# Optimization experiments

Measured on AMD Instinct MI355X. Metric: run time of the kernel, lower is better.

The kernel has to match this reference:

```python
import jax, jax.numpy as jnp
import numpy as np

L = 10   # lattice side (hardcoded self.length)
K = 3    # kernel_size -> half_k = 1 wrap padding
FN = 4   # filter_num
B = 262144


def setup_inputs() -> dict:
    key = jax.random.key(0)
    k1, k2, k3, k4, k5 = jax.random.split(key, 5)
    v = jax.random.normal(k1, (B, L * L), dtype=jnp.float32)
    # torch default init scale ~ 1/sqrt(fan_in)
    conv_w = jax.random.normal(k2, (FN, 1, K, K), dtype=jnp.float32) / 3.0
    conv_b = jax.random.normal(k3, (FN,), dtype=jnp.float32) * 0.1
    deconv_w = jax.random.normal(k4, (FN, 1, 2, 2), dtype=jnp.float32) / 4.0
    deconv_b = jax.random.normal(k5, (1,), dtype=jnp.float32) * 0.1
    data = jnp.zeros((1,), dtype=jnp.int32)  # unused positional arg of log_psi
    return {"v": v, "conv_w": conv_w, "conv_b": conv_b,
            "deconv_w": deconv_w, "deconv_b": deconv_b, "data": data}


def _log_psi(v, conv_w, conv_b, deconv_w, deconv_b):
    b = v.shape[0]
    x = v.reshape(b, 1, L, L)
    # handmade_padding == periodic (wrap) pad of width half_k=1 on both spatial axes
    x = jnp.pad(x, ((0, 0), (0, 0), (1, 1), (1, 1)), mode="wrap")  # [B,1,12,12]
    # Conv2d(1, FN, 3), VALID -> [B,FN,10,10]
    y = jax.lax.conv_general_dilated(
        x, conv_w, window_strides=(1, 1), padding="VALID",
        dimension_numbers=("NCHW", "OIHW", "NCHW"))
    y = y + conv_b[None, :, None, None]
    # MaxPool2d(2,2): non-overlapping 2x2 -> [B,FN,5,5]
    y = y.reshape(b, FN, L // 2, 2, L // 2, 2).max(axis=(3, 5))
    # ConvTranspose2d(FN,1,kernel=2,stride=2): each input pixel -> disjoint 2x2 block
    # torch weight layout [in=FN, out=1, 2, 2]
    z = jnp.einsum("bcij,cokl->boikjl", y, deconv_w).reshape(b, 1, L, L)
    z = z + deconv_b[None, :, None, None]
    sign_z = jnp.sign(z)
    abs_z = z * sign_z
    sign_prod = sign_z.reshape(b, -1).prod(axis=1)        # scalar per sample
    log_sum = jnp.log(abs_z).reshape(b, -1).sum(axis=1)   # scalar per sample
    return sign_prod, log_sum


def reference(v, conv_w, conv_b, deconv_w, deconv_b, data):
    return _log_psi(v, conv_w, conv_b, deconv_w, deconv_b)
```

## Files before the change

kernel.cpp:

```cpp
#include <hip/hip_runtime.h>
#include <math.h>

__global__ __launch_bounds__(256) void CNN2D_37495064494620_kernel(
    const float* __restrict__ v,
    const float* __restrict__ cw,
    const float* __restrict__ cb,
    const float* __restrict__ dw,
    const float* __restrict__ db,
    float* __restrict__ out,
    int B)
{
    const int b = blockIdx.x * 256 + threadIdx.x;
    if (b >= B) return;

    float W[4][9];
    #pragma unroll
    for (int f = 0; f < 4; ++f)
        #pragma unroll
        for (int t = 0; t < 9; ++t)
            W[f][t] = cw[f * 9 + t];
    float Cb[4];
    #pragma unroll
    for (int f = 0; f < 4; ++f) Cb[f] = cb[f];
    float Dw[4][4];
    #pragma unroll
    for (int f = 0; f < 4; ++f)
        #pragma unroll
        for (int t = 0; t < 4; ++t)
            Dw[f][t] = dw[f * 4 + t];
    const float Db = db[0];

    float X[100];
    const float4* src = (const float4*)(v + (size_t)b * 100);
    #pragma unroll
    for (int t = 0; t < 25; ++t) {
        float4 q = src[t];
        X[4 * t + 0] = q.x;
        X[4 * t + 1] = q.y;
        X[4 * t + 2] = q.z;
        X[4 * t + 3] = q.w;
    }

    unsigned sbits = 0u;
    float l2 = 0.0f;

    #pragma unroll
    for (int i = 0; i < 5; ++i) {
        #pragma unroll
        for (int j = 0; j < 5; ++j) {
            float p0, p1, p2, p3;
            #pragma unroll
            for (int dr = 0; dr < 2; ++dr) {
                #pragma unroll
                for (int dc = 0; dc < 2; ++dc) {
                    const int r = 2 * i + dr, c = 2 * j + dc;
                    float a0 = Cb[0], a1 = Cb[1], a2 = Cb[2], a3 = Cb[3];
                    #pragma unroll
                    for (int kr = 0; kr < 3; ++kr) {
                        const int rr = (r + kr + 9) % 10;
                        #pragma unroll
                        for (int kc = 0; kc < 3; ++kc) {
                            const int cc = (c + kc + 9) % 10;
                            const float xv = X[rr * 10 + cc];
                            const int t = kr * 3 + kc;
                            a0 = fmaf(xv, W[0][t], a0);
                            a1 = fmaf(xv, W[1][t], a1);
                            a2 = fmaf(xv, W[2][t], a2);
                            a3 = fmaf(xv, W[3][t], a3);
                        }
                    }
                    if (dr == 0 && dc == 0) {
                        p0 = a0; p1 = a1; p2 = a2; p3 = a3;
                    } else {
                        p0 = fmaxf(p0, a0); p1 = fmaxf(p1, a1);
                        p2 = fmaxf(p2, a2); p3 = fmaxf(p3, a3);
                    }
                }
            }
            float z[4];
            #pragma unroll
            for (int kl = 0; kl < 4; ++kl) {
                float zz = Db;
                zz = fmaf(p0, Dw[0][kl], zz);
                zz = fmaf(p1, Dw[1][kl], zz);
                zz = fmaf(p2, Dw[2][kl], zz);
                zz = fmaf(p3, Dw[3][kl], zz);
                z[kl] = zz;
                sbits ^= __float_as_uint(zz);
            }
            l2 += __log2f(fabsf(z[0] * z[1])) + __log2f(fabsf(z[2] * z[3]));
        }
    }

    out[b]     = (sbits & 0x80000000u) ? -1.0f : 1.0f;
    out[B + b] = l2 * 0.69314718055994531f;
}

extern "C" void kernel_launch(void* const* d_in, const int* in_sizes, int n_in,
                              void* d_out, int out_size, void* d_ws, size_t ws_size,
                              hipStream_t stream) {
    const float* v  = (const float*)d_in[0];
    const float* cw = (const float*)d_in[1];
    const float* cb = (const float*)d_in[2];
    const float* dw = (const float*)d_in[3];
    const float* db = (const float*)d_in[4];
    float* out = (float*)d_out;

    const int B = in_sizes[0] / 100;
    const int grid = (B + 255) / 256;
    CNN2D_37495064494620_kernel<<<grid, 256, 0, stream>>>(v, cw, cb, dw, db, out, B);
}
```

Before: 171.3 us.

## Stream input rows in pairs and broadcast weights via readfirstlane

Instead of loading all 100 floats of a sample into registers up front, the kernel loads the lattice in 20-float row-pair chunks and processes one pooled row at a time. It reloads the second row-pair for the wrap-around so fewer values need to stay live at once. Weights and biases are passed through readfirstlane so they can sit in scalar registers instead of per-lane VGPRs. The aim is lower VGPR pressure and higher occupancy, at the cost of one redundant 80-byte global load per sample.

After: 174.1 us. No clear change (+1.6%).

```diff
diff --git a/kernel.cpp b/kernel.cpp
--- a/kernel.cpp
+++ b/kernel.cpp
@@ -1,5 +1,79 @@
 #include <hip/hip_runtime.h>
 #include <math.h>
+
+
+#define SREAD(x) __int_as_float(__builtin_amdgcn_readfirstlane(__float_as_int(x)))
+
+__device__ __forceinline__ void load_pair(float (&P)[20], const float* base) {
+    const float4* s = (const float4*)base;
+    #pragma unroll
+    for (int t = 0; t < 5; ++t) {
+        float4 q = s[t];
+        P[4 * t + 0] = q.x;
+        P[4 * t + 1] = q.y;
+        P[4 * t + 2] = q.z;
+        P[4 * t + 3] = q.w;
+    }
+}
+
+__device__ __forceinline__ void pool_row(
+    const float (&pa)[20], const float (&pb)[20], const float (&pc)[20],
+    const float (&W)[4][9], const float (&Cb)[4], const float (&Dw)[4][4],
+    const float Db, const int j2base ,
+    unsigned& sbits, float& l2)
+{
+    (void)j2base;
+    float Xw[4][10];
+    #pragma unroll
+    for (int c = 0; c < 10; ++c) {
+        Xw[0][c] = pa[10 + c];
+        Xw[1][c] = pb[c];
+        Xw[2][c] = pb[10 + c];
+        Xw[3][c] = pc[c];
+    }
+    #pragma unroll
+    for (int j = 0; j < 5; ++j) {
+        float p0, p1, p2, p3;
+        #pragma unroll
+        for (int dr = 0; dr < 2; ++dr) {
+            #pragma unroll
+            for (int dc = 0; dc < 2; ++dc) {
+                float a0 = Cb[0], a1 = Cb[1], a2 = Cb[2], a3 = Cb[3];
+                #pragma unroll
+                for (int kr = 0; kr < 3; ++kr) {
+                    #pragma unroll
+                    for (int kc = 0; kc < 3; ++kc) {
+                        const int cc = (2 * j + dc + kc + 9) % 10;
+                        const float xv = Xw[dr + kr][cc];
+                        const int t = kr * 3 + kc;
+                        a0 = fmaf(xv, W[0][t], a0);
+                        a1 = fmaf(xv, W[1][t], a1);
+                        a2 = fmaf(xv, W[2][t], a2);
+                        a3 = fmaf(xv, W[3][t], a3);
+                    }
+                }
+                if (dr == 0 && dc == 0) {
+                    p0 = a0; p1 = a1; p2 = a2; p3 = a3;
+                } else {
+                    p0 = fmaxf(p0, a0); p1 = fmaxf(p1, a1);
+                    p2 = fmaxf(p2, a2); p3 = fmaxf(p3, a3);
+                }
+            }
+        }
+        float z[4];
+        #pragma unroll
+        for (int kl = 0; kl < 4; ++kl) {
+            float zz = Db;
+            zz = fmaf(p0, Dw[0][kl], zz);
+            zz = fmaf(p1, Dw[1][kl], zz);
+            zz = fmaf(p2, Dw[2][kl], zz);
+            zz = fmaf(p3, Dw[3][kl], zz);
+            z[kl] = zz;
+            sbits ^= __float_as_uint(zz);
+        }
+        l2 += __log2f(fabsf(z[0] * z[1])) + __log2f(fabsf(z[2] * z[3]));
+    }
+}
 
 __global__ __launch_bounds__(256) void CNN2D_37495064494620_kernel(
     const float* __restrict__ v,
@@ -18,79 +92,43 @@
     for (int f = 0; f < 4; ++f)
         #pragma unroll
         for (int t = 0; t < 9; ++t)
-            W[f][t] = cw[f * 9 + t];
+            W[f][t] = SREAD(cw[f * 9 + t]);
     float Cb[4];
     #pragma unroll
-    for (int f = 0; f < 4; ++f) Cb[f] = cb[f];
+    for (int f = 0; f < 4; ++f) Cb[f] = SREAD(cb[f]);
     float Dw[4][4];
     #pragma unroll
     for (int f = 0; f < 4; ++f)
         #pragma unroll
         for (int t = 0; t < 4; ++t)
-            Dw[f][t] = dw[f * 4 + t];
-    const float Db = db[0];
+            Dw[f][t] = SREAD(dw[f * 4 + t]);
+    const float Db = SREAD(db[0]);
 
-    float X[100];
-    const float4* src = (const float4*)(v + (size_t)b * 100);
-    #pragma unroll
-    for (int t = 0; t < 25; ++t) {
-        float4 q = src[t];
-        X[4 * t + 0] = q.x;
-        X[4 * t + 1] = q.y;
-        X[4 * t + 2] = q.z;
-        X[4 * t + 3] = q.w;
-    }
+    const float* src = v + (size_t)b * 100;
 
     unsigned sbits = 0u;
     float l2 = 0.0f;
 
-    #pragma unroll
-    for (int i = 0; i < 5; ++i) {
-        #pragma unroll
-        for (int j = 0; j < 5; ++j) {
-            float p0, p1, p2, p3;
-            #pragma unroll
-            for (int dr = 0; dr < 2; ++dr) {
-                #pragma unroll
-                for (int dc = 0; dc < 2; ++dc) {
-                    const int r = 2 * i + dr, c = 2 * j + dc;
-                    float a0 = Cb[0], a1 = Cb[1], a2 = Cb[2], a3 = Cb[3];
-                    #pragma unroll
-                    for (int kr = 0; kr < 3; ++kr) {
-                        const int rr = (r + kr + 9) % 10;
-                        #pragma unroll
-                        for (int kc = 0; kc < 3; ++kc) {
-                            const int cc = (c + kc + 9) % 10;
-                            const float xv = X[rr * 10 + cc];
-                            const int t = kr * 3 + kc;
-                            a0 = fmaf(xv, W[0][t], a0);
-                            a1 = fmaf(xv, W[1][t], a1);
-                            a2 = fmaf(xv, W[2][t], a2);
-                            a3 = fmaf(xv, W[3][t], a3);
-                        }
-                    }
-                    if (dr == 0 && dc == 0) {
-                        p0 = a0; p1 = a1; p2 = a2; p3 = a3;
-                    } else {
-                        p0 = fmaxf(p0, a0); p1 = fmaxf(p1, a1);
-                        p2 = fmaxf(p2, a2); p3 = fmaxf(p3, a3);
-                    }
-                }
-            }
-            float z[4];
-            #pragma unroll
-            for (int kl = 0; kl < 4; ++kl) {
-                float zz = Db;
-                zz = fmaf(p0, Dw[0][kl], zz);
-                zz = fmaf(p1, Dw[1][kl], zz);
-                zz = fmaf(p2, Dw[2][kl], zz);
-                zz = fmaf(p3, Dw[3][kl], zz);
-                z[kl] = zz;
-                sbits ^= __float_as_uint(zz);
-            }
-            l2 += __log2f(fabsf(z[0] * z[1])) + __log2f(fabsf(z[2] * z[3]));
-        }
-    }
+    float P0[20], P1[20], P2[20], P3[20], P4[20], P1b[20];
+
+    load_pair(P0, src + 0);
+    load_pair(P1, src + 20);
+    load_pair(P2, src + 40);
+    load_pair(P3, src + 60);
+
+    pool_row(P0, P1, P2, W, Cb, Dw, Db, 0, sbits, l2);
+
+    load_pair(P4, src + 80);
+
+    pool_row(P1, P2, P3, W, Cb, Dw, Db, 0, sbits, l2);
+
+    pool_row(P2, P3, P4, W, Cb, Dw, Db, 0, sbits, l2);
+
+    load_pair(P1b, src + 20);
+
+    pool_row(P3, P4, P0, W, Cb, Dw, Db, 0, sbits, l2);
+
+    pool_row(P4, P0, P1b, W, Cb, Dw, Db, 0, sbits, l2);
 
     out[b]     = (sbits & 0x80000000u) ? -1.0f : 1.0f;
     out[B + b] = l2 * 0.69314718055994531f;
```

## Stage inputs through LDS with async global_load_lds and stream rows per output row

Applied to the files above, without the earlier changes.

Each block now copies its 128 samples into shared memory with coalesced global_load_lds transfers, instead of having every thread issue strided float4 loads of its own 100-float sample. The compute loop over output rows is no longer unrolled and reads only the 4 needed rows per iteration from LDS. This cuts register pressure from the 100-element array and should raise occupancy. Weights are made wave-uniform via readfirstlane, and the block size drops to 128. The risks are 50KB of LDS per block limiting resident blocks, bank conflicts from the stride-100 per-thread reads, and the removal of the B bounds check.

Result: slower. 182.2 us (+6.4%).

```diff
diff --git a/kernel.cpp b/kernel.cpp
--- a/kernel.cpp
+++ b/kernel.cpp
@@ -1,7 +1,10 @@
 #include <hip/hip_runtime.h>
 #include <math.h>
 
-__global__ __launch_bounds__(256) void CNN2D_37495064494620_kernel(
+
+#define SREAD(x) __int_as_float(__builtin_amdgcn_readfirstlane(__float_as_int(x)))
+
+__global__ __launch_bounds__(128) void CNN2D_37495064494620_kernel(
     const float* __restrict__ v,
     const float* __restrict__ cw,
     const float* __restrict__ cb,
@@ -10,42 +13,61 @@
     float* __restrict__ out,
     int B)
 {
-    const int b = blockIdx.x * 256 + threadIdx.x;
-    if (b >= B) return;
+    const int tid = threadIdx.x;
+    const int b = blockIdx.x * 128 + tid;
+
+    __shared__ __align__(16) float sm[128 * 100];
+
+    const float* gbase = v + (size_t)blockIdx.x * 12800;
+    const int widx = tid >> 6;
+    #pragma unroll
+    for (int k = 0; k < 25; ++k) {
+        __builtin_amdgcn_global_load_lds(
+            (const __attribute__((address_space(1))) void*)(gbase + k * 512 + tid * 4),
+            (__attribute__((address_space(3))) void*)&sm[k * 512 + widx * 256],
+            16, 0, 0);
+    }
 
     float W[4][9];
     #pragma unroll
     for (int f = 0; f < 4; ++f)
         #pragma unroll
         for (int t = 0; t < 9; ++t)
-            W[f][t] = cw[f * 9 + t];
+            W[f][t] = SREAD(cw[f * 9 + t]);
     float Cb[4];
     #pragma unroll
-    for (int f = 0; f < 4; ++f) Cb[f] = cb[f];
+    for (int f = 0; f < 4; ++f) Cb[f] = SREAD(cb[f]);
     float Dw[4][4];
     #pragma unroll
     for (int f = 0; f < 4; ++f)
         #pragma unroll
         for (int t = 0; t < 4; ++t)
-            Dw[f][t] = dw[f * 4 + t];
-    const float Db = db[0];
+            Dw[f][t] = SREAD(dw[f * 4 + t]);
+    const float Db = SREAD(db[0]);
 
-    float X[100];
-    const float4* src = (const float4*)(v + (size_t)b * 100);
-    #pragma unroll
-    for (int t = 0; t < 25; ++t) {
-        float4 q = src[t];
-        X[4 * t + 0] = q.x;
-        X[4 * t + 1] = q.y;
-        X[4 * t + 2] = q.z;
-        X[4 * t + 3] = q.w;
-    }
+    __syncthreads();
 
+    const int myoff = tid * 100;
     unsigned sbits = 0u;
     float l2 = 0.0f;
 
-    #pragma unroll
+    #pragma clang loop unroll(disable)
     for (int i = 0; i < 5; ++i) {
+        const int rows[4] = { (i == 0) ? 9 : 2 * i - 1,
+                              2 * i,
+                              2 * i + 1,
+                              (i == 4) ? 0 : 2 * i + 2 };
+        float R[4][10];
+        #pragma unroll
+        for (int rr = 0; rr < 4; ++rr) {
+            const int base = myoff + rows[rr] * 10;
+            #pragma unroll
+            for (int t = 0; t < 5; ++t) {
+                float2 q = *(const float2*)&sm[base + 2 * t];
+                R[rr][2 * t]     = q.x;
+                R[rr][2 * t + 1] = q.y;
+            }
+        }
         #pragma unroll
         for (int j = 0; j < 5; ++j) {
             float p0, p1, p2, p3;
@@ -53,15 +75,13 @@
             for (int dr = 0; dr < 2; ++dr) {
                 #pragma unroll
                 for (int dc = 0; dc < 2; ++dc) {
-                    const int r = 2 * i + dr, c = 2 * j + dc;
                     float a0 = Cb[0], a1 = Cb[1], a2 = Cb[2], a3 = Cb[3];
                     #pragma unroll
                     for (int kr = 0; kr < 3; ++kr) {
-                        const int rr = (r + kr + 9) % 10;
                         #pragma unroll
                         for (int kc = 0; kc < 3; ++kc) {
-                            const int cc = (c + kc + 9) % 10;
-                            const float xv = X[rr * 10 + cc];
+                            const int cc = (2 * j + dc + kc + 9) % 10;
+                            const float xv = R[dr + kr][cc];
                             const int t = kr * 3 + kc;
                             a0 = fmaf(xv, W[0][t], a0);
                             a1 = fmaf(xv, W[1][t], a1);
@@ -107,6 +127,6 @@
     float* out = (float*)d_out;
 
     const int B = in_sizes[0] / 100;
-    const int grid = (B + 255) / 256;
-    CNN2D_37495064494620_kernel<<<grid, 256, 0, stream>>>(v, cw, cb, dw, db, out, B);
+    const int grid = (B + 127) / 128;
+    CNN2D_37495064494620_kernel<<<grid, 128, 0, stream>>>(v, cw, cb, dw, db, out, B);
 }
```
